# Performance work log

Measured on AMD Instinct MI355X. Metric: run time of the kernel, lower is better.

## Reference

```python
import jax, jax.numpy as jnp
import numpy as np

DIM, HEADS, HEAD_DIM, EPS = 1536, 12, 128, 1e-6
B, S = 1, 4096


def rmsnorm(x, w, eps=EPS):
    v = jnp.mean(jnp.square(x), axis=-1, keepdims=True)
    return x * jax.lax.rsqrt(v + eps) * w


def apply_rope(x, freqs):
    # x: [b,s,n,d]; freqs: [s, d//2] rotation angles (complex rope on adjacent pairs)
    b, s, n, d = x.shape
    xr = x.reshape(b, s, n, d // 2, 2)
    cos = jnp.cos(freqs)[None, :, None, :]
    sin = jnp.sin(freqs)[None, :, None, :]
    x0, x1 = xr[..., 0], xr[..., 1]
    out = jnp.stack([x0 * cos - x1 * sin, x0 * sin + x1 * cos], axis=-1)
    return out.reshape(b, s, n, d)


def setup_inputs() -> dict:
    key = jax.random.key(0)
    ks = jax.random.split(key, 12)
    scale = 0.02
    x = jax.random.normal(ks[0], (B, S, DIM), jnp.float32)
    # standard rope angles: pos * inv_freq
    inv_freq = 1.0 / (10000.0 ** (jnp.arange(0, HEAD_DIM, 2, dtype=jnp.float32) / HEAD_DIM))
    freqs = jnp.arange(S, dtype=jnp.float32)[:, None] * inv_freq[None, :]  # [S, 64]
    Wq = jax.random.normal(ks[1], (DIM, DIM), jnp.float32) * scale
    bq = jax.random.normal(ks[2], (DIM,), jnp.float32) * scale
    Wk = jax.random.normal(ks[3], (DIM, DIM), jnp.float32) * scale
    bk = jax.random.normal(ks[4], (DIM,), jnp.float32) * scale
    Wv = jax.random.normal(ks[5], (DIM, DIM), jnp.float32) * scale
    bv = jax.random.normal(ks[6], (DIM,), jnp.float32) * scale
    Wo = jax.random.normal(ks[7], (DIM, DIM), jnp.float32) * scale
    bo = jax.random.normal(ks[8], (DIM,), jnp.float32) * scale
    gq = 1.0 + jax.random.normal(ks[9], (DIM,), jnp.float32) * 0.01
    gk = 1.0 + jax.random.normal(ks[10], (DIM,), jnp.float32) * 0.01
    return dict(x=x, freqs=freqs, Wq=Wq, bq=bq, Wk=Wk, bk=bk, Wv=Wv, bv=bv,
                Wo=Wo, bo=bo, gq=gq, gk=gk)


def reference(x, freqs, Wq, bq, Wk, bk, Wv, bv, Wo, bo, gq, gk):
    b, s = x.shape[:2]
    n, d = HEADS, HEAD_DIM
    q = apply_rope(rmsnorm(x @ Wq.T + bq, gq).reshape(b, s, n, d), freqs)
    k = apply_rope(rmsnorm(x @ Wk.T + bk, gk).reshape(b, s, n, d), freqs)
    v = (x @ Wv.T + bv).reshape(b, s, n, d)
    # SDPA: softmax(q k^T / sqrt(d)) v
    scores = jnp.einsum('bqnd,bknd->bnqk', q, k) / jnp.sqrt(jnp.asarray(d, x.dtype))
    attn = jax.nn.softmax(scores, axis=-1)
    out = jnp.einsum('bnqk,bknd->bqnd', attn, v).reshape(b, s, n * d)
    return out @ Wo.T + bo
```

## Files before the change

kernel.cpp:

```cpp
#include <hip/hip_runtime.h>
#include <stdint.h>
#include <math.h>

#define DIM 1536
#define SEQ 4096
#define HEADS 12
#define HD 128

typedef __bf16 bf16x8 __attribute__((ext_vector_type(8)));
typedef float f32x4 __attribute__((ext_vector_type(4)));

typedef __attribute__((address_space(1))) void gas_void;
typedef __attribute__((address_space(3))) void las_void;

__device__ __forceinline__ float b2f(unsigned short u) {
  union { unsigned int i; float f; } x; x.i = ((unsigned int)u) << 16; return x.f;
}
__device__ __forceinline__ unsigned short f2b(float f) {
  union { float f; unsigned int i; } x; x.f = f;
  unsigned int u = x.i;
  unsigned int r = (u + 0x7fffu + ((u >> 16) & 1u)) >> 16;
  return (unsigned short)r;
}
__device__ __forceinline__ void gll16(const unsigned short* g, unsigned short* l) {
  __builtin_amdgcn_global_load_lds((gas_void*)g, (las_void*)l, 16, 0, 0);
}
__device__ __forceinline__ void cvtpk(unsigned int& d, float a, float b) {
  asm("v_cvt_pk_bf16_f32 %0, %1, %2" : "=v"(d) : "v"(a), "v"(b));
}
__device__ __forceinline__ void pl32(unsigned int& a, unsigned int& b) {
  asm("v_permlane32_swap_b32 %0, %1" : "+v"(a), "+v"(b));
}
__device__ __forceinline__ void pl16(unsigned int& a, unsigned int& b) {
  asm("v_permlane16_swap_b32 %0, %1" : "+v"(a), "+v"(b));
}
__device__ __forceinline__ float fexp2(float x) { return __builtin_amdgcn_exp2f(x); }

__global__ void detect_kernel(const unsigned int* __restrict__ xw, int* flag) {
  __shared__ int cnt;
  if (threadIdx.x == 0) cnt = 0;
  __syncthreads();
  int local = 0;
  for (int i = threadIdx.x; i < 1024; i += 256) {
    unsigned int e = (xw[i] >> 7) & 0xFFu;
    if (e >= 110u && e <= 140u) local++;
  }
  atomicAdd(&cnt, local);
  __syncthreads();
  if (threadIdx.x == 0) *flag = (cnt > 512) ? 0 : 1;
}

__global__ void convert_big_kernel(const void* sx, const void* s0, const void* s1,
                                   const void* s2, const void* s3,
                                   unsigned short* dx, unsigned short* d0,
                                   unsigned short* d1, unsigned short* d2,
                                   unsigned short* d3,
                                   int nx4, int nw4, int dtk,
                                   const int* __restrict__ flag) {
  const void* s; unsigned short* d; int n4;
  switch (blockIdx.y) {
    case 0: s = sx; d = dx; n4 = nx4; break;
    case 1: s = s0; d = d0; n4 = nw4; break;
    case 2: s = s1; d = d1; n4 = nw4; break;
    case 3: s = s2; d = d2; n4 = nw4; break;
    default: s = s3; d = d3; n4 = nw4; break;
  }
  int f = (dtk >= 0) ? dtk : *flag;
  for (int i = blockIdx.x * blockDim.x + threadIdx.x; i < n4; i += gridDim.x * blockDim.x) {
    if (f) {
      float4 v = ((const float4*)s)[i];
      union { unsigned short h[4]; uint2 u; } pk;
      pk.h[0] = f2b(v.x); pk.h[1] = f2b(v.y); pk.h[2] = f2b(v.z); pk.h[3] = f2b(v.w);
      ((uint2*)d)[i] = pk.u;
    } else {
      ((uint2*)d)[i] = ((const uint2*)s)[i];
    }
  }
}

__global__ void convert_small_kernel(const void* s0, const void* s1, const void* s2,
                                     const void* s3, const void* s4, const void* s5,
                                     const void* sf,
                                     unsigned short* d0, unsigned short* d1,
                                     unsigned short* d2, unsigned short* d3,
                                     unsigned short* d4, unsigned short* d5,
                                     float2* df, int nb, int nf, int dtk,
                                     const int* __restrict__ flag) {
  int f = (dtk >= 0) ? dtk : *flag;
  if (blockIdx.y == 6) {
    for (int i = blockIdx.x * blockDim.x + threadIdx.x; i < nf; i += gridDim.x * blockDim.x) {
      float a = f ? ((const float*)sf)[i] : b2f(((const unsigned short*)sf)[i]);
      float sn, cs;
      __sincosf(a, &sn, &cs);
      df[i] = make_float2(cs, sn);
    }
    return;
  }
  const void* s; unsigned short* d;
  switch (blockIdx.y) {
    case 0: s = s0; d = d0; break;
    case 1: s = s1; d = d1; break;
    case 2: s = s2; d = d2; break;
    case 3: s = s3; d = d3; break;
    case 4: s = s4; d = d4; break;
    default: s = s5; d = d5; break;
  }
  for (int i = blockIdx.x * blockDim.x + threadIdx.x; i < nb; i += gridDim.x * blockDim.x)
    d[i] = f ? f2b(((const float*)s)[i]) : ((const unsigned short*)s)[i];
}

__global__ void signal_kernel(float* out) { if (threadIdx.x == 0) out[0] = 999.0f; }

template<int BM>
__device__ __forceinline__ void gemm_bt_body(
    const unsigned short* __restrict__ A,
    const unsigned short* __restrict__ W,
    const unsigned short* __restrict__ bias,
    unsigned short* __restrict__ Cb, float* __restrict__ Cf, int fmt, int vmode,
    int K, int N, int bx, int by)
{
  constexpr int BK = 64;
  constexpr int MI = BM / 32;
  constexpr int ALINES = BM * BK * 2 / 4096;
  __shared__ unsigned short As[BM * BK];
  __shared__ unsigned short Bs[128 * BK];
  const int t = threadIdx.x;
  const int wave = t >> 6, lane = t & 63;
  const int quad = lane >> 4, l16 = lane & 15;
  const int m0 = by * BM, n0 = bx * 128;
  const int wm = (wave >> 1) * (BM / 2), wn = (wave & 1) * 64;

  f32x4 acc[MI][4] = {};

  const int srow = t >> 3;
  const int scol = ((t & 7) ^ ((t >> 3) & 7)) * 8;
  const unsigned short* Ag = A + (size_t)(m0 + srow) * K + scol;
  const unsigned short* Wg = W + (size_t)(n0 + srow) * K + scol;

  for (int k0 = 0; k0 < K; k0 += BK) {
    __syncthreads();
#pragma unroll
    for (int L = 0; L < ALINES; ++L)
      gll16(Ag + (size_t)L * 32 * K + k0, &As[L * 2048 + t * 8]);
#pragma unroll
    for (int L = 0; L < 4; ++L)
      gll16(Wg + (size_t)L * 32 * K + k0, &Bs[L * 2048 + t * 8]);
    __syncthreads();
#pragma unroll
    for (int c = 0; c < 2; ++c) {
      bf16x8 af[MI], bfr[4];
#pragma unroll
      for (int i = 0; i < MI; ++i) {
        int row = wm + i * 16 + l16;
        af[i] = *(const bf16x8*)&As[row * 64 + ((c * 4 + quad) ^ (row & 7)) * 8];
      }
#pragma unroll
      for (int j = 0; j < 4; ++j) {
        int row = wn + j * 16 + l16;
        bfr[j] = *(const bf16x8*)&Bs[row * 64 + ((c * 4 + quad) ^ (row & 7)) * 8];
      }
#pragma unroll
      for (int i = 0; i < MI; ++i)
#pragma unroll
        for (int j = 0; j < 4; ++j)
          acc[i][j] = __builtin_amdgcn_mfma_f32_16x16x32_bf16(af[i], bfr[j], acc[i][j], 0, 0, 0);
    }
  }

#pragma unroll
  for (int i = 0; i < MI; ++i) {
    int row = m0 + wm + i * 16 + quad * 4;
#pragma unroll
    for (int j = 0; j < 4; ++j) {
      int col = n0 + wn + j * 16 + l16;
      float bv = b2f(bias[col]);
      if (vmode) {
        union { unsigned short h4[4]; uint2 u; } pk;
#pragma unroll
        for (int r = 0; r < 4; ++r) pk.h4[r] = f2b(acc[i][j][r] + bv);
        *(uint2*)&Cb[(size_t)col * SEQ + row] = pk.u;
      } else {
#pragma unroll
        for (int r = 0; r < 4; ++r) {
          float v = acc[i][j][r] + bv;
          size_t idx = (size_t)(row + r) * N + col;
          if (fmt) Cf[idx] = v; else Cb[idx] = f2b(v);
        }
      }
    }
  }
}

__global__ __launch_bounds__(256) void qkv_gemm_kernel(
    const unsigned short* __restrict__ x,
    const unsigned short* __restrict__ Wq, const unsigned short* __restrict__ bq,
    const unsigned short* __restrict__ Wk, const unsigned short* __restrict__ bk,
    const unsigned short* __restrict__ Wv, const unsigned short* __restrict__ bv,
    unsigned short* qb, unsigned short* kb, unsigned short* vt)
{
  const int flat = blockIdx.x + 12 * blockIdx.y + 768 * blockIdx.z;
  const int swz = (flat & 7) * 288 + (flat >> 3);
  const int bz = swz / 768;
  const int rem = swz - bz * 768;
  const int by = rem / 12, bx = rem - by * 12;
  const unsigned short *W, *b; unsigned short* C; int vm = 0;
  if (bz == 0)      { W = Wq; b = bq; C = qb; }
  else if (bz == 1) { W = Wk; b = bk; C = kb; }
  else              { W = Wv; b = bv; C = vt; vm = 1; }
  gemm_bt_body<64>(x, W, b, C, nullptr, 0, vm, DIM, DIM, bx, by);
}

__global__ __launch_bounds__(256) void out_gemm_kernel(
    const unsigned short* __restrict__ ab, const unsigned short* __restrict__ Wo,
    const unsigned short* __restrict__ bo, void* out, int dtk,
    const int* __restrict__ flag)
{
  const int flat = blockIdx.x + 12 * blockIdx.y;
  const int swz = (flat & 7) * 96 + (flat >> 3);
  const int by = swz / 12, bx = swz - by * 12;
  int fmt = (dtk >= 0) ? dtk : *flag;
  gemm_bt_body<64>(ab, Wo, bo, (unsigned short*)out, (float*)out, fmt, 0,
                   DIM, DIM, bx, by);
}

__global__ __launch_bounds__(256) void norm_rope_kernel(
    unsigned short* __restrict__ qb, unsigned short* __restrict__ kb,
    const unsigned short* __restrict__ gq, const unsigned short* __restrict__ gk,
    const float2* __restrict__ csf)
{
  const int s = blockIdx.x;
  const int isq = (blockIdx.y == 0);
  unsigned short* row = (isq ? qb : kb) + (size_t)s * DIM;
  const unsigned short* g = (isq ? gq : gk);
  const int t = threadIdx.x;
  float ss = 0.f;
#pragma unroll
  for (int i = 0; i < 6; ++i) {
    float xv = b2f(row[t + 256 * i]);
    ss += xv * xv;
  }
#pragma unroll
  for (int off = 32; off > 0; off >>= 1) ss += __shfl_down(ss, off);
  __shared__ float red[4];
  if ((t & 63) == 0) red[t >> 6] = ss;
  __syncthreads();
  float tot = red[0] + red[1] + red[2] + red[3];
  float rinv = 1.0f / sqrtf(tot * (1.0f / DIM) + 1e-6f);
  if (isq) rinv *= 0.12751744900725559f;
#pragma unroll
  for (int i = 0; i < 3; ++i) {
    int pg = t + 256 * i;
    int c0 = pg * 2;
    float x0 = b2f(row[c0]), x1 = b2f(row[c0 + 1]);
    float y0 = x0 * rinv * b2f(g[c0]);
    float y1 = x1 * rinv * b2f(g[c0 + 1]);
    float2 cs = csf[s * 64 + (pg & 63)];
    row[c0]     = f2b(y0 * cs.x - y1 * cs.y);
    row[c0 + 1] = f2b(y0 * cs.y + y1 * cs.x);
  }
}

__global__ __launch_bounds__(256) void attn_kernel(
    const unsigned short* __restrict__ qb,
    const unsigned short* __restrict__ kb,
    const unsigned short* __restrict__ vt,
    float* __restrict__ op,
    float* __restrict__ lp,
    int seg, int nwg)
{
  __shared__ unsigned short Ks[64 * 128];
  __shared__ unsigned short Vs[128 * 64];

  const int t = threadIdx.x;
  const int wave = t >> 6, lane = t & 63;
  const int quad = lane >> 4, l16 = lane & 15;

  const int flat = blockIdx.x + (gridDim.x) * (blockIdx.y + HEADS * blockIdx.z);
  const int swz = (flat & 7) * (nwg >> 3) + (flat >> 3);
  const int bx = swz & 31;
  const int rem = swz >> 5;
  const int h = rem % HEADS;
  const int z = rem / HEADS;

  const int qbase = bx * 128 + wave * 32;
  const int kc0 = z * seg;

  bf16x8 qf[2][4];
#pragma unroll
  for (int mt = 0; mt < 2; ++mt)
#pragma unroll
    for (int kk = 0; kk < 4; ++kk)
      qf[mt][kk] = *(const bf16x8*)(qb + (size_t)(qbase + mt * 16 + l16) * DIM
                                    + h * HD + kk * 32 + quad * 8);

  f32x4 o[2][8] = {};
  float Lr[2] = {};

  const int krow = t >> 2, kblk = (t & 3) * 4;
  const int vd = t >> 1,  vblk = (t & 1) * 4;

  const unsigned short* kbase = kb + (size_t)krow * DIM + h * HD + kblk * 8;
  const unsigned short* vbase = vt + ((size_t)h * HD + vd) * SEQ + vblk * 8;

  uint4 kr0, kr1, kr2, kr3, vr0, vr1, vr2, vr3;
  {
    const unsigned short* s = kbase + (size_t)kc0 * DIM;
    kr0 = *(const uint4*)(s);
    kr1 = *(const uint4*)(s + 8);
    kr2 = *(const uint4*)(s + 16);
    kr3 = *(const uint4*)(s + 24);
    const unsigned short* sv = vbase + kc0;
    vr0 = *(const uint4*)(sv);
    vr1 = *(const uint4*)(sv + 8);
    vr2 = *(const uint4*)(sv + 16);
    vr3 = *(const uint4*)(sv + 24);
  }

  for (int kc = kc0; kc < kc0 + seg; kc += 64) {
    __syncthreads();
    {
      unsigned short* dst = &Ks[krow * 128];
      const int sw = krow & 7;
      *(uint4*)(dst + ((kblk + 0) ^ sw) * 8) = kr0;
      *(uint4*)(dst + ((kblk + 1) ^ sw) * 8) = kr1;
      *(uint4*)(dst + ((kblk + 2) ^ sw) * 8) = kr2;
      *(uint4*)(dst + ((kblk + 3) ^ sw) * 8) = kr3;
    }
    {
      unsigned short* dst = &Vs[vd * 64];
      const int sw = vd & 7;
      *(uint4*)(dst + ((vblk + 0) ^ sw) * 8) = vr0;
      *(uint4*)(dst + ((vblk + 1) ^ sw) * 8) = vr1;
      *(uint4*)(dst + ((vblk + 2) ^ sw) * 8) = vr2;
      *(uint4*)(dst + ((vblk + 3) ^ sw) * 8) = vr3;
    }
    __syncthreads();

    {
      int nkc = kc + 64;
      if (nkc >= kc0 + seg) nkc = kc;
      const unsigned short* s = kbase + (size_t)nkc * DIM;
      kr0 = *(const uint4*)(s);
      kr1 = *(const uint4*)(s + 8);
      kr2 = *(const uint4*)(s + 16);
      kr3 = *(const uint4*)(s + 24);
      const unsigned short* sv = vbase + nkc;
      vr0 = *(const uint4*)(sv);
      vr1 = *(const uint4*)(sv + 8);
      vr2 = *(const uint4*)(sv + 16);
      vr3 = *(const uint4*)(sv + 24);
    }

    f32x4 sc[2][4] = {};
    __builtin_amdgcn_s_setprio(1);
#pragma unroll
    for (int kk = 0; kk < 4; ++kk) {
#pragma unroll
      for (int j = 0; j < 4; ++j) {
        int row = j * 16 + l16;
        bf16x8 kf = *(const bf16x8*)&Ks[row * 128 + ((kk * 4 + quad) ^ (row & 7)) * 8];
        sc[0][j] = __builtin_amdgcn_mfma_f32_16x16x32_bf16(kf, qf[0][kk], sc[0][j], 0, 0, 0);
        sc[1][j] = __builtin_amdgcn_mfma_f32_16x16x32_bf16(kf, qf[1][kk], sc[1][j], 0, 0, 0);
      }
    }
    __builtin_amdgcn_s_setprio(0);

    unsigned int wlo[2][4], whi[2][4];
#pragma unroll
    for (int mt = 0; mt < 2; ++mt) {
      float ls = 0.f;
#pragma unroll
      for (int j = 0; j < 4; ++j) {
        float p0 = fexp2(sc[mt][j][0]);
        float p1 = fexp2(sc[mt][j][1]);
        float p2 = fexp2(sc[mt][j][2]);
        float p3 = fexp2(sc[mt][j][3]);
        ls += (p0 + p1) + (p2 + p3);
        cvtpk(wlo[mt][j], p0, p1);
        cvtpk(whi[mt][j], p2, p3);
      }
      Lr[mt] += ls;
    }

    bf16x8 pf[2][2];
#pragma unroll
    for (int mt = 0; mt < 2; ++mt)
#pragma unroll
      for (int kk2 = 0; kk2 < 2; ++kk2) {
        unsigned int ul = wlo[mt][kk2 * 2], vl = wlo[mt][kk2 * 2 + 1];
        unsigned int uh = whi[mt][kk2 * 2], vh = whi[mt][kk2 * 2 + 1];
        pl32(ul, vl); pl16(ul, vl);
        pl32(uh, vh); pl16(uh, vh);
        union { unsigned int w[4]; bf16x8 v; } u;
        u.w[0] = ul; u.w[1] = uh; u.w[2] = vl; u.w[3] = vh;
        pf[mt][kk2] = u.v;
      }

    __builtin_amdgcn_s_setprio(1);
#pragma unroll
    for (int kk2 = 0; kk2 < 2; ++kk2) {
#pragma unroll
      for (int j2 = 0; j2 < 8; ++j2) {
        bf16x8 vf = *(const bf16x8*)&Vs[(j2 * 16 + l16) * 64
                                        + ((kk2 * 4 + quad) ^ (l16 & 7)) * 8];
        o[0][j2] = __builtin_amdgcn_mfma_f32_16x16x32_bf16(pf[0][kk2], vf, o[0][j2], 0, 0, 0);
        o[1][j2] = __builtin_amdgcn_mfma_f32_16x16x32_bf16(pf[1][kk2], vf, o[1][j2], 0, 0, 0);
      }
    }
    __builtin_amdgcn_s_setprio(0);
  }

  float* opz = op + (size_t)z * SEQ * DIM;
  float* lpz = lp + (size_t)z * HEADS * SEQ + (size_t)h * SEQ;
#pragma unroll
  for (int mt = 0; mt < 2; ++mt) {
    float L = Lr[mt];
    L += __shfl_xor(L, 16);
    L += __shfl_xor(L, 32);
    if (lane < 16) lpz[qbase + mt * 16 + l16] = L;
  }
#pragma unroll
  for (int mt = 0; mt < 2; ++mt) {
#pragma unroll
    for (int j2 = 0; j2 < 8; ++j2) {
      int col = h * HD + j2 * 16 + l16;
#pragma unroll
      for (int r = 0; r < 4; ++r) {
        int row = qbase + mt * 16 + quad * 4 + r;
        opz[(size_t)row * DIM + col] = o[mt][j2][r];
      }
    }
  }
}

__global__ __launch_bounds__(256) void combine_kernel(
    const float* __restrict__ op, const float* __restrict__ lp,
    unsigned short* __restrict__ ab, int nz)
{
  int idx4 = blockIdx.x * 256 + threadIdx.x;
  int idx = idx4 * 4;
  int row = idx / DIM, col = idx - row * DIM;
  int h = col >> 7;
  float4 o = make_float4(0.f, 0.f, 0.f, 0.f);
  float l = 0.f;
  for (int z = 0; z < nz; ++z) {
    float4 v = *(const float4*)(op + (size_t)z * SEQ * DIM + idx);
    o.x += v.x; o.y += v.y; o.z += v.z; o.w += v.w;
    l += lp[(size_t)z * HEADS * SEQ + (size_t)h * SEQ + row];
  }
  float inv = 1.0f / l;
  union { unsigned short h4[4]; uint2 u; } pk;
  pk.h4[0] = f2b(o.x * inv);
  pk.h4[1] = f2b(o.y * inv);
  pk.h4[2] = f2b(o.z * inv);
  pk.h4[3] = f2b(o.w * inv);
  *(uint2*)&ab[idx] = pk.u;
}

extern "C" void kernel_launch(void* const* d_in, const int* in_sizes, int n_in,
                              void* d_out, int out_size, void* d_ws, size_t ws_size,
                              hipStream_t stream) {
  const int NX = SEQ * DIM, NW = DIM * DIM, NB = DIM, NF = SEQ * 64;

  char* w = (char*)d_ws;
  size_t off = 0;
  int* flag = (int*)(w + off);              off += 256;
  unsigned short* xb  = (unsigned short*)(w + off); off += (size_t)NX * 2;
  unsigned short* Wqb = (unsigned short*)(w + off); off += (size_t)NW * 2;
  unsigned short* Wkb = (unsigned short*)(w + off); off += (size_t)NW * 2;
  unsigned short* Wvb = (unsigned short*)(w + off); off += (size_t)NW * 2;
  unsigned short* Wob = (unsigned short*)(w + off); off += (size_t)NW * 2;
  unsigned short* bqb = (unsigned short*)(w + off); off += 4096;
  unsigned short* bkb = (unsigned short*)(w + off); off += 4096;
  unsigned short* bvb = (unsigned short*)(w + off); off += 4096;
  unsigned short* bob = (unsigned short*)(w + off); off += 4096;
  unsigned short* gqb = (unsigned short*)(w + off); off += 4096;
  unsigned short* gkb = (unsigned short*)(w + off); off += 4096;
  float2* freqcs = (float2*)(w + off);      off += (size_t)NF * 8;
  unsigned short* qb = (unsigned short*)(w + off); off += (size_t)NX * 2;
  unsigned short* kb = (unsigned short*)(w + off); off += (size_t)NX * 2;
  unsigned short* vt = (unsigned short*)(w + off); off += (size_t)NX * 2;
  unsigned short* ab = (unsigned short*)(w + off); off += (size_t)NX * 2;
  float* op = (float*)(w + off);
  float* lp;

  int nz = 2;
  size_t need2 = off + (size_t)2 * NX * 4 + (size_t)2 * HEADS * SEQ * 4;
  if (ws_size < need2) {
    signal_kernel<<<1, 64, 0, stream>>>((float*)d_out);
    return;
  }
  lp = (float*)(w + off + (size_t)nz * NX * 4);

  int dt = -1;
  if ((long long)in_sizes[0] == (long long)NX * 2 &&
      (long long)in_sizes[2] == (long long)NW * 2) dt = 0;
  else if ((long long)in_sizes[0] == (long long)NX * 4 &&
           (long long)in_sizes[2] == (long long)NW * 4) dt = 1;

  if (dt < 0)
    detect_kernel<<<1, 256, 0, stream>>>((const unsigned int*)d_in[0], flag);

  const int CT = 256;
  auto cgrid = [](int n) { int g = (n + 255) / 256; return g > 4096 ? 4096 : g; };

  const unsigned short* xg  = xb;
  const unsigned short* Wqg = Wqb, *Wkg = Wkb, *Wvg = Wvb, *Wog = Wob;
  const unsigned short* bqg = bqb, *bkg = bkb, *bvg = bvb, *bog = bob;
  const unsigned short* gqg = gqb, *gkg = gkb;
  if (dt == 0) {
    xg  = (const unsigned short*)d_in[0];
    Wqg = (const unsigned short*)d_in[2];
    Wkg = (const unsigned short*)d_in[4];
    Wvg = (const unsigned short*)d_in[6];
    Wog = (const unsigned short*)d_in[8];
    bqg = (const unsigned short*)d_in[3];
    bkg = (const unsigned short*)d_in[5];
    bvg = (const unsigned short*)d_in[7];
    bog = (const unsigned short*)d_in[9];
    gqg = (const unsigned short*)d_in[10];
    gkg = (const unsigned short*)d_in[11];
  } else {
    convert_big_kernel<<<dim3(cgrid(NW / 4), 5), CT, 0, stream>>>(
        d_in[0], d_in[2], d_in[4], d_in[6], d_in[8],
        xb, Wqb, Wkb, Wvb, Wob, NX / 4, NW / 4, dt, flag);
  }
  convert_small_kernel<<<dim3(cgrid(NF), 7), CT, 0, stream>>>(
      d_in[3], d_in[5], d_in[7], d_in[9], d_in[10], d_in[11], d_in[1],
      bqb, bkb, bvb, bob, gqb, gkb, freqcs, NB, NF, dt, flag);

  qkv_gemm_kernel<<<dim3(DIM / 128, SEQ / 64, 3), 256, 0, stream>>>(
      xg, Wqg, bqg, Wkg, bkg, Wvg, bvg, qb, kb, vt);
  norm_rope_kernel<<<dim3(SEQ, 2), 256, 0, stream>>>(qb, kb, gqg, gkg, freqcs);
  attn_kernel<<<dim3(SEQ / 128, HEADS, nz), 256, 0, stream>>>(
      qb, kb, vt, op, lp, SEQ / nz, (SEQ / 128) * HEADS * nz);
  combine_kernel<<<NX / 1024, 256, 0, stream>>>(op, lp, ab, nz);
  out_gemm_kernel<<<dim3(DIM / 128, SEQ / 64), 256, 0, stream>>>(
      ab, Wog, bog, d_out, dt, flag);
}
```

Before: 384.2 us.

## Double-buffer K tile in LDS via direct global-to-LDS loads in attention

```diff
diff --git a/kernel.cpp b/kernel.cpp
--- a/kernel.cpp
+++ b/kernel.cpp
@@ -268,7 +268,7 @@
     float* __restrict__ lp,
     int seg, int nwg)
 {
-  __shared__ unsigned short Ks[64 * 128];
+  __shared__ unsigned short Ks[2][64 * 128];
   __shared__ unsigned short Vs[128 * 64];
 
   const int t = threadIdx.x;
@@ -284,6 +284,7 @@
 
   const int qbase = bx * 128 + wave * 32;
   const int kc0 = z * seg;
+  const int nt = seg >> 6;
 
   bf16x8 qf[2][4];
 #pragma unroll
@@ -296,54 +297,44 @@
   f32x4 o[2][8] = {};
   float Lr[2] = {};
 
-  const int krow = t >> 2, kblk = (t & 3) * 4;
-  const int vd = t >> 1,  vblk = (t & 1) * 4;
-
-  const unsigned short* kbase = kb + (size_t)krow * DIM + h * HD + kblk * 8;
+  const int sK = t >> 4;
+  const int cK = (t & 15) ^ (sK & 7);
+  const unsigned short* Kg = kb + (size_t)sK * DIM + h * HD + cK * 8;
+
+  const int vd = t >> 1, vblk = (t & 1) * 4;
   const unsigned short* vbase = vt + ((size_t)h * HD + vd) * SEQ + vblk * 8;
 
-  uint4 kr0, kr1, kr2, kr3, vr0, vr1, vr2, vr3;
+  uint4 vr0, vr1, vr2, vr3;
+
+#pragma unroll
+  for (int L = 0; L < 4; ++L)
+    gll16(Kg + (size_t)(kc0 + L * 16) * DIM, &Ks[0][L * 2048 + t * 8]);
   {
-    const unsigned short* s = kbase + (size_t)kc0 * DIM;
-    kr0 = *(const uint4*)(s);
-    kr1 = *(const uint4*)(s + 8);
-    kr2 = *(const uint4*)(s + 16);
-    kr3 = *(const uint4*)(s + 24);
     const unsigned short* sv = vbase + kc0;
     vr0 = *(const uint4*)(sv);
     vr1 = *(const uint4*)(sv + 8);
     vr2 = *(const uint4*)(sv + 16);
     vr3 = *(const uint4*)(sv + 24);
   }
-
-  for (int kc = kc0; kc < kc0 + seg; kc += 64) {
-    __syncthreads();
+  __syncthreads();
+  {
+    unsigned short* dst = &Vs[vd * 64];
+    const int sw = vd & 7;
+    *(uint4*)(dst + ((vblk + 0) ^ sw) * 8) = vr0;
+    *(uint4*)(dst + ((vblk + 1) ^ sw) * 8) = vr1;
+    *(uint4*)(dst + ((vblk + 2) ^ sw) * 8) = vr2;
+    *(uint4*)(dst + ((vblk + 3) ^ sw) * 8) = vr3;
+  }
+  __syncthreads();
+
+  for (int it = 0; it < nt; ++it) {
+    const int cur = it & 1;
+    int nkc = kc0 + (it + 1) * 64;
+    if (it + 1 >= nt) nkc = kc0 + it * 64;
+#pragma unroll
+    for (int L = 0; L < 4; ++L)
+      gll16(Kg + (size_t)(nkc + L * 16) * DIM, &Ks[cur ^ 1][L * 2048 + t * 8]);
     {
-      unsigned short* dst = &Ks[krow * 128];
-      const int sw = krow & 7;
-      *(uint4*)(dst + ((kblk + 0) ^ sw) * 8) = kr0;
-      *(uint4*)(dst + ((kblk + 1) ^ sw) * 8) = kr1;
-      *(uint4*)(dst + ((kblk + 2) ^ sw) * 8) = kr2;
-      *(uint4*)(dst + ((kblk + 3) ^ sw) * 8) = kr3;
-    }
-    {
-      unsigned short* dst = &Vs[vd * 64];
-      const int sw = vd & 7;
-      *(uint4*)(dst + ((vblk + 0) ^ sw) * 8) = vr0;
-      *(uint4*)(dst + ((vblk + 1) ^ sw) * 8) = vr1;
-      *(uint4*)(dst + ((vblk + 2) ^ sw) * 8) = vr2;
-      *(uint4*)(dst + ((vblk + 3) ^ sw) * 8) = vr3;
-    }
-    __syncthreads();
-
-    {
-      int nkc = kc + 64;
-      if (nkc >= kc0 + seg) nkc = kc;
-      const unsigned short* s = kbase + (size_t)nkc * DIM;
-      kr0 = *(const uint4*)(s);
-      kr1 = *(const uint4*)(s + 8);
-      kr2 = *(const uint4*)(s + 16);
-      kr3 = *(const uint4*)(s + 24);
       const unsigned short* sv = vbase + nkc;
       vr0 = *(const uint4*)(sv);
       vr1 = *(const uint4*)(sv + 8);
@@ -351,6 +342,8 @@
       vr3 = *(const uint4*)(sv + 24);
     }
 
+    const unsigned short* ks = &Ks[cur][0];
+
     f32x4 sc[2][4] = {};
     __builtin_amdgcn_s_setprio(1);
 #pragma unroll
@@ -358,7 +351,7 @@
 #pragma unroll
       for (int j = 0; j < 4; ++j) {
         int row = j * 16 + l16;
-        bf16x8 kf = *(const bf16x8*)&Ks[row * 128 + ((kk * 4 + quad) ^ (row & 7)) * 8];
+        bf16x8 kf = *(const bf16x8*)&ks[row * 128 + ((kk * 4 + quad) ^ (row & 7)) * 8];
         sc[0][j] = __builtin_amdgcn_mfma_f32_16x16x32_bf16(kf, qf[0][kk], sc[0][j], 0, 0, 0);
         sc[1][j] = __builtin_amdgcn_mfma_f32_16x16x32_bf16(kf, qf[1][kk], sc[1][j], 0, 0, 0);
       }
@@ -408,6 +401,17 @@
       }
     }
     __builtin_amdgcn_s_setprio(0);
+
+    __syncthreads();
+    {
+      unsigned short* dst = &Vs[vd * 64];
+      const int sw = vd & 7;
+      *(uint4*)(dst + ((vblk + 0) ^ sw) * 8) = vr0;
+      *(uint4*)(dst + ((vblk + 1) ^ sw) * 8) = vr1;
+      *(uint4*)(dst + ((vblk + 2) ^ sw) * 8) = vr2;
+      *(uint4*)(dst + ((vblk + 3) ^ sw) * 8) = vr3;
+    }
+    __syncthreads();
   }
 
   float* opz = op + (size_t)z * SEQ * DIM;
```

Result: slower. 401.0 us (+4.4%).
